# Performance work log

Measured on AMD Instinct MI355X. Metric: run time of the kernel, lower is better.

## Reference

```python
import jax, jax.numpy as jnp
import numpy as np

B, N = 4, 512
H, NH, L = 64, 4, 3
HD = H // NH          # 16
NODE_F, EDGE_F = 18, 7
H4 = H // 4           # 16
FF = 4 * H            # 256


def _ln(x, g, b, eps=1e-5):
    m = jnp.mean(x, axis=-1, keepdims=True)
    v = jnp.mean((x - m) ** 2, axis=-1, keepdims=True)
    return (x - m) * jax.lax.rsqrt(v + eps) * g + b


def _leaky(x):
    return jnp.where(x >= 0, x, 0.2 * x)


def _spd(edge_mask):
    # Vectorized Floyd-Warshall, mirrors GraphTransformer._compute_spd_matrix
    n = edge_mask.shape[1]
    spd = jnp.where(edge_mask, 1.0, float(n)).astype(jnp.float32)
    i = jnp.arange(n)
    spd = spd.at[:, i, i].set(0.0)
    def body(k, s):
        col = jax.lax.dynamic_slice_in_dim(s, k, 1, axis=2)  # [B,N,1]
        row = jax.lax.dynamic_slice_in_dim(s, k, 1, axis=1)  # [B,1,N]
        return jnp.minimum(s, col + row)
    return jax.lax.fori_loop(0, n, body, spd)


def setup_inputs() -> dict:
    key = jax.random.key(0)
    ks = iter(jax.random.split(key, 64))
    def nrm(shape, s):
        return jax.random.normal(next(ks), shape, jnp.float32) * s
    inp = {}
    inp["node_features"] = jax.random.normal(next(ks), (B, N, NODE_F), jnp.float32)
    inp["edge_features"] = jax.random.normal(next(ks), (B, N, N, EDGE_F), jnp.float32)
    nm = jax.random.uniform(next(ks), (B, N)) < 0.9
    inp["node_mask"] = nm.at[:, 0].set(True)
    inp["edge_mask"] = jax.random.uniform(next(ks), (B, N, N)) < 0.05
    s_h = 1.0 / np.sqrt(H)
    inp["node_proj_w"] = nrm((NODE_F, H), 0.2)
    inp["node_proj_b"] = jnp.zeros((H,), jnp.float32)
    inp["edge_proj_w"] = nrm((EDGE_F, H), 0.2)
    inp["edge_proj_b"] = jnp.zeros((H,), jnp.float32)
    inp["wq"] = nrm((L, H, H), s_h)
    inp["wk"] = nrm((L, H, H), s_h)
    inp["wv"] = nrm((L, H, H), s_h)
    inp["eb1_w"] = nrm((L, H, H4), s_h)
    inp["eb1_b"] = jnp.zeros((L, H4), jnp.float32)
    inp["eb_ln_g"] = jnp.ones((L, H4), jnp.float32)
    inp["eb_ln_b"] = jnp.zeros((L, H4), jnp.float32)
    inp["eb2_w"] = nrm((L, H4, NH), 0.2)
    inp["eb2_b"] = jnp.zeros((L, NH), jnp.float32)
    inp["spd1_w"] = nrm((L, 1, H4), 0.5)
    inp["spd1_b"] = jnp.zeros((L, H4), jnp.float32)
    inp["spd2_w"] = nrm((L, H4, NH), 0.2)
    inp["spd2_b"] = jnp.zeros((L, NH), jnp.float32)
    inp["wo_w"] = nrm((L, H, H), s_h)
    inp["wo_b"] = jnp.zeros((L, H), jnp.float32)
    inp["ln1_g"] = jnp.ones((L, H), jnp.float32)
    inp["ln1_b"] = jnp.zeros((L, H), jnp.float32)
    inp["ln2_g"] = jnp.ones((L, H), jnp.float32)
    inp["ln2_b"] = jnp.zeros((L, H), jnp.float32)
    inp["ffn1_w"] = nrm((L, H, FF), s_h)
    inp["ffn1_b"] = jnp.zeros((L, FF), jnp.float32)
    inp["ffn2_w"] = nrm((L, FF, H), 1.0 / np.sqrt(FF))
    inp["ffn2_b"] = jnp.zeros((L, H), jnp.float32)
    inp["score1_w"] = nrm((2 * H, H), 1.0 / np.sqrt(2 * H))
    inp["score1_b"] = jnp.zeros((H,), jnp.float32)
    inp["score_ln_g"] = jnp.ones((H,), jnp.float32)
    inp["score_ln_b"] = jnp.zeros((H,), jnp.float32)
    inp["score2_w"] = nrm((H, 1), 0.1)
    inp["score2_b"] = jnp.zeros((1,), jnp.float32)
    return inp


def reference(node_features, edge_features, node_mask, edge_mask,
              node_proj_w, node_proj_b, edge_proj_w, edge_proj_b,
              wq, wk, wv,
              eb1_w, eb1_b, eb_ln_g, eb_ln_b, eb2_w, eb2_b,
              spd1_w, spd1_b, spd2_w, spd2_b,
              wo_w, wo_b, ln1_g, ln1_b, ln2_g, ln2_b,
              ffn1_w, ffn1_b, ffn2_w, ffn2_b,
              score1_w, score1_b, score_ln_g, score_ln_b, score2_w, score2_b):
    NEG = -1000000000.0
    h = node_features @ node_proj_w + node_proj_b            # [B,N,H]
    e = edge_features @ edge_proj_w + edge_proj_b            # [B,N,N,H]
    spd = _spd(edge_mask)
    spd_n = (jnp.clip(spd, 0.0, 10.0) / 10.0)[..., None]      # [B,N,N,1]
    scale = 1.0 / np.sqrt(HD)
    for l in range(L):
        Q = (h @ wq[l]).reshape(B, N, NH, HD)
        K = (h @ wk[l]).reshape(B, N, NH, HD)
        V = (h @ wv[l]).reshape(B, N, NH, HD)
        scores = jnp.einsum('bihd,bjhd->bhij', Q, K) * scale  # [B,NH,N,N]
        x = _leaky(_ln(e @ eb1_w[l] + eb1_b[l], eb_ln_g[l], eb_ln_b[l]))
        edge_bias = jnp.transpose(x @ eb2_w[l] + eb2_b[l], (0, 3, 1, 2))
        sb = _leaky(spd_n @ spd1_w[l] + spd1_b[l]) @ spd2_w[l] + spd2_b[l]
        spd_bias = jnp.transpose(sb, (0, 3, 1, 2))
        bias = jnp.where(edge_mask[:, None, :, :], edge_bias, spd_bias)
        scores = jnp.where(node_mask[:, None, None, :], scores + bias, NEG)
        attn = jax.nn.softmax(scores, axis=-1)
        out = jnp.einsum('bhij,bjhd->bihd', attn, V).reshape(B, N, H)
        out = out @ wo_w[l] + wo_b[l]
        h = _ln(h + out, ln1_g[l], ln1_b[l])
        ff = jax.nn.gelu(h @ ffn1_w[l] + ffn1_b[l], approximate=False) @ ffn2_w[l] + ffn2_b[l]
        h = _ln(h + ff, ln2_g[l], ln2_b[l])
    h_ego = jnp.broadcast_to(h[:, :1, :], (B, N - 1, H))
    hc = jnp.concatenate([h_ego, h[:, 1:, :]], axis=-1)       # [B,N-1,2H]
    x = _leaky(_ln(hc @ score1_w + score1_b, score_ln_g, score_ln_b))
    logits = (x @ score2_w + score2_b)[..., 0]                # [B,N-1]
    cand_mask = node_mask[:, 1:]
    no_cand = ~jnp.any(cand_mask, axis=-1)
    cand_mask = cand_mask.at[:, 0].set(cand_mask[:, 0] | no_cand)
    logits = jnp.where(cand_mask, logits, NEG)
    probs = jax.nn.softmax(logits, axis=-1)
    return probs, h
```

## Files before the change

kernel.cpp:

```cpp
#include <hip/hip_runtime.h>
#include <math.h>

#define BB 4
#define NN 512
#define HH 64
#define NHH 4
#define HDD 16
#define LL 3
#define NNSQ 262144
#define FFF 256

__device__ __forceinline__ float wsum(float x) {
#pragma unroll
    for (int o = 1; o < 64; o <<= 1) x += __shfl_xor(x, o);
    return x;
}
__device__ __forceinline__ float wmaxr(float x) {
#pragma unroll
    for (int o = 1; o < 64; o <<= 1) x = fmaxf(x, __shfl_xor(x, o));
    return x;
}

__global__ void k_adj(const int* __restrict__ em, unsigned long long* __restrict__ adj,
                      unsigned int* __restrict__ blockCnt) {
    __shared__ unsigned int wc[4];
    int wv = threadIdx.x >> 6, lane = threadIdx.x & 63;
    int wid = blockIdx.x * 4 + wv;
    int chunk = wid & 7;
    int row = wid >> 3;
    int j = chunk * 64 + lane;
    int v = em[(size_t)row * NN + j];
    unsigned long long bal = __ballot(v != 0);
    if (lane == 0) { adj[row * 8 + chunk] = bal; wc[wv] = (unsigned int)__popcll(bal); }
    __syncthreads();
    if (threadIdx.x == 0) blockCnt[blockIdx.x] = wc[0] + wc[1] + wc[2] + wc[3];
}

__global__ void k_bfs(const unsigned long long* __restrict__ adj, unsigned char* __restrict__ spd) {
    __shared__ unsigned long long vis[8], fro[8], nxt[8];
    __shared__ unsigned long long dist8[64];
    unsigned char* dist = (unsigned char*)dist8;
    int t = threadIdx.x;
    int row = blockIdx.x;
    int b = row >> 9; int src = row & 511;
    dist8[t] = 0x0A0A0A0A0A0A0A0AULL;
    if (t < 8) { vis[t] = 0ULL; fro[t] = 0ULL; }
    __syncthreads();
    if (t == 0) {
        dist[src] = 0;
        vis[src >> 6] = 1ULL << (src & 63);
        fro[src >> 6] = 1ULL << (src & 63);
    }
    __syncthreads();
    const unsigned long long* arow = adj + (size_t)b * NN * 8;
    for (int d = 1; d <= 9; d++) {
        if (t < 8) nxt[t] = 0ULL;
        __syncthreads();
        int c = t >> 3, w = t & 7;
        unsigned long long f = fro[c];
        unsigned long long acc = 0ULL;
        while (f) {
            int k = (c << 6) + __builtin_ctzll(f);
            f &= f - 1;
            acc |= arow[k * 8 + w];
        }
        if (acc) atomicOr(&nxt[w], acc);
        __syncthreads();
        if (t < 8) {
            unsigned long long nw = nxt[t] & ~vis[t];
            vis[t] |= nw;
            fro[t] = nw;
            while (nw) {
                int j = (t << 6) + __builtin_ctzll(nw);
                nw &= nw - 1;
                dist[j] = (unsigned char)d;
            }
        }
        __syncthreads();
    }
    ((unsigned long long*)(spd + (size_t)row * NN))[t] = dist8[t];
}

__global__ __launch_bounds__(1024) void k_scan(const unsigned int* __restrict__ blockCnt,
                                               unsigned int* __restrict__ blockOff,
                                               unsigned int* __restrict__ counter) {
    __shared__ unsigned int part[1024];
    int t = threadIdx.x;
    unsigned int v0 = blockCnt[t * 4], v1 = blockCnt[t * 4 + 1],
                 v2 = blockCnt[t * 4 + 2], v3 = blockCnt[t * 4 + 3];
    unsigned int s = v0 + v1 + v2 + v3;
    part[t] = s;
    __syncthreads();
    for (int o = 1; o < 1024; o <<= 1) {
        unsigned int add = (t >= o) ? part[t - o] : 0u;
        __syncthreads();
        part[t] += add;
        __syncthreads();
    }
    unsigned int excl = part[t] - s;
    blockOff[t * 4]     = excl;
    blockOff[t * 4 + 1] = excl + v0;
    blockOff[t * 4 + 2] = excl + v0 + v1;
    blockOff[t * 4 + 3] = excl + v0 + v1 + v2;
    if (t == 1023) { counter[0] = part[t]; blockOff[4096] = part[t]; }
}

__global__ void k_scatter(const int* __restrict__ em, const unsigned int* __restrict__ blockOff,
                          unsigned int* __restrict__ elist) {
    __shared__ unsigned int wc[4];
    int t = threadIdx.x; int lane = t & 63; int wv = t >> 6;
    int idx = blockIdx.x * 256 + t;
    bool m = em[idx] != 0;
    unsigned long long bal = __ballot(m);
    if (lane == 0) wc[wv] = (unsigned int)__popcll(bal);
    __syncthreads();
    unsigned int base = blockOff[blockIdx.x];
    for (int w = 0; w < wv; w++) base += wc[w];
    if (m) {
        int pre = __popcll(bal & ((1ULL << lane) - 1ULL));
        elist[base + pre] = (unsigned int)idx;
    }
}

__global__ __launch_bounds__(256) void k_edge_bias(
    const float* __restrict__ ef, const unsigned int* __restrict__ counter,
    const unsigned int* __restrict__ elist,
    const float* __restrict__ epw, const float* __restrict__ epb,
    const float* __restrict__ eb1w, const float* __restrict__ eb1b,
    const float* __restrict__ lng, const float* __restrict__ lnb,
    const float* __restrict__ eb2w, const float* __restrict__ eb2b,
    float* __restrict__ vals) {
    unsigned int count = *counter;
    unsigned int idx = blockIdx.x * 256 + threadIdx.x;
    if (idx >= count) return;
    int l = blockIdx.y;
    unsigned int pos = elist[idx];
    const float* e7 = ef + (size_t)pos * 7;
    float f0 = e7[0], f1 = e7[1], f2 = e7[2], f3 = e7[3], f4 = e7[4], f5 = e7[5], f6 = e7[6];
    float tt[16];
#pragma unroll
    for (int c = 0; c < 16; c++) tt[c] = eb1b[l * 16 + c];
    const float* W1 = eb1w + l * 1024;
    for (int k = 0; k < 64; k++) {
        float ek = epb[k] + f0 * epw[k] + f1 * epw[64 + k] + f2 * epw[128 + k] + f3 * epw[192 + k]
                 + f4 * epw[256 + k] + f5 * epw[320 + k] + f6 * epw[384 + k];
#pragma unroll
        for (int c = 0; c < 16; c++) tt[c] += ek * W1[k * 16 + c];
    }
    float m = 0.f;
#pragma unroll
    for (int c = 0; c < 16; c++) m += tt[c];
    m *= 0.0625f;
    float var = 0.f;
#pragma unroll
    for (int c = 0; c < 16; c++) { float d = tt[c] - m; var += d * d; }
    var *= 0.0625f;
    float inv = rsqrtf(var + 1e-5f);
#pragma unroll
    for (int c = 0; c < 16; c++) {
        float x = (tt[c] - m) * inv * lng[l * 16 + c] + lnb[l * 16 + c];
        tt[c] = x >= 0.f ? x : 0.2f * x;
    }
#pragma unroll
    for (int hh = 0; hh < 4; hh++) {
        float a = eb2b[l * 4 + hh];
#pragma unroll
        for (int c = 0; c < 16; c++) a += tt[c] * eb2w[(l * 16 + c) * 4 + hh];
        vals[(unsigned int)((l * 4 + hh) << 16) + idx] = a;
    }
}

__global__ void k_node_proj(const float* __restrict__ nf, const float* __restrict__ w,
                            const float* __restrict__ bb, float* __restrict__ h) {
    int wid = blockIdx.x * 4 + (threadIdx.x >> 6);
    int f = threadIdx.x & 63;
    const float* r = nf + (size_t)wid * 18;
    float acc = bb[f];
#pragma unroll
    for (int c = 0; c < 18; c++) acc += r[c] * w[c * 64 + f];
    h[(size_t)wid * 64 + f] = acc;
}

__global__ __launch_bounds__(256) void k_qkvT(
    const float* __restrict__ h,
    const float* __restrict__ WQ, const float* __restrict__ WK, const float* __restrict__ WV,
    float* __restrict__ Q, float* __restrict__ KT, float* __restrict__ VT) {
    __shared__ float h_lds[16][64];
    int t = threadIdx.x;
    size_t base = (size_t)blockIdx.x * 16 * 64;
    for (int u = t; u < 1024; u += 256) ((float*)h_lds)[u] = h[base + u];
    __syncthreads();
    int wv = t >> 6, lane = t & 63;
    float aq[4] = {0,0,0,0}, ak[4] = {0,0,0,0}, av[4] = {0,0,0,0};
    for (int k = 0; k < 64; k++) {
        float wqv = WQ[k * 64 + lane], wkv = WK[k * 64 + lane], wvv = WV[k * 64 + lane];
#pragma unroll
        for (int r = 0; r < 4; r++) {
            float hv = h_lds[wv * 4 + r][k];
            aq[r] += hv * wqv; ak[r] += hv * wkv; av[r] += hv * wvv;
        }
    }
#pragma unroll
    for (int r = 0; r < 4; r++) {
        Q[base + (size_t)(wv * 4 + r) * 64 + lane] = aq[r];
    }
    int b = blockIdx.x >> 5;
    int j0 = (blockIdx.x & 31) * 16 + wv * 4;
    float4 kk; kk.x = ak[0]; kk.y = ak[1]; kk.z = ak[2]; kk.w = ak[3];
    float4 vv; vv.x = av[0]; vv.y = av[1]; vv.z = av[2]; vv.w = av[3];
    *(float4*)(KT + ((size_t)(b * 64 + lane)) * 512 + j0) = kk;
    *(float4*)(VT + ((size_t)(b * 64 + lane)) * 512 + j0) = vv;
}

__global__ __launch_bounds__(256) void k_attn3(
    const float* __restrict__ Q, const float* __restrict__ KT, const float* __restrict__ VT,
    const unsigned char* __restrict__ spd, const unsigned int* __restrict__ elist,
    const unsigned int* __restrict__ rowOff, const float* __restrict__ vals,
    const float* __restrict__ s1w, const float* __restrict__ s1b,
    const float* __restrict__ s2w, const float* __restrict__ s2b,
    const int* __restrict__ nmask, int l, float* __restrict__ attO) {
    __shared__ float kt[8192];
    __shared__ float bv[8192];
    __shared__ float tab[11];
    int bh = blockIdx.x;
    int b  = bh >> 2, hh = bh & 3;
    int i0 = blockIdx.y * 16;
    int t = threadIdx.x, wv = t >> 6, lane = t & 63;
    int rbase = i0 + wv * 4;
    float qv = Q[((size_t)(b * 512 + rbase + (lane >> 4))) * 64 + hh * 16 + (lane & 15)];
    float q[4][16];
#pragma unroll
    for (int r = 0; r < 4; r++)
#pragma unroll
        for (int d = 0; d < 16; d++)
            q[r][d] = __shfl(qv, r * 16 + d);
    const float4* ktg = (const float4*)(KT + (size_t)bh * 8192);
    float4* kts = (float4*)kt;
#pragma unroll
    for (int u = 0; u < 8; u++) kts[t + u * 256] = ktg[t + u * 256];
    if (t < 11) {
        float x = (float)t * 0.1f;
        float acc = s2b[l * 4 + hh];
#pragma unroll
        for (int c = 0; c < 16; c++) {
            float v = x * s1w[l * 16 + c] + s1b[l * 16 + c];
            v = v >= 0.f ? v : 0.2f * v;
            acc += v * s2w[(l * 16 + c) * 4 + hh];
        }
        tab[t] = acc;
    }
    __syncthreads();
    const unsigned char* sp = spd + ((size_t)(b * 512 + i0)) * 512;
#pragma unroll
    for (int u = 0; u < 8; u++) {
        int e4 = u * 1024 + t * 4;
        unsigned int w4 = *(const unsigned int*)(sp + e4);
        bv[e4 + 0] = tab[w4 & 255u];
        bv[e4 + 1] = tab[(w4 >> 8) & 255u];
        bv[e4 + 2] = tab[(w4 >> 16) & 255u];
        bv[e4 + 3] = tab[w4 >> 24];
    }
    __syncthreads();
    unsigned int vplane = (unsigned int)((l * 4 + hh) << 16);
#pragma unroll
    for (int rr = 0; rr < 4; rr++) {
        int g = b * 512 + rbase + rr;
        unsigned int e0 = rowOff[2 * g], e1 = rowOff[2 * g + 2];
        for (unsigned int e = e0 + lane; e < e1; e += 64) {
            int j = (int)(elist[e] & 511u);
            bv[(wv * 4 + rr) * 512 + j] = vals[vplane + e];
        }
    }
    __syncthreads();
    const int* nmb = nmask + b * 512;
    float sc[8][4];
    float mx[4] = {-3e38f, -3e38f, -3e38f, -3e38f};
#pragma unroll
    for (int c = 0; c < 8; c++) {
        int j = c * 64 + lane;
        float ktv[16];
#pragma unroll
        for (int d = 0; d < 16; d++) ktv[d] = kt[d * 512 + j];
        float madd = (nmb[j] != 0) ? 0.f : -1e9f;
#pragma unroll
        for (int r = 0; r < 4; r++) {
            float s = 0.f;
#pragma unroll
            for (int d = 0; d < 16; d++) s += q[r][d] * ktv[d];
            s = s * 0.25f + bv[(wv * 4 + r) * 512 + j] + madd;
            sc[c][r] = s;
            mx[r] = fmaxf(mx[r], s);
        }
    }
#pragma unroll
    for (int r = 0; r < 4; r++) mx[r] = wmaxr(mx[r]);
    float sm[4] = {0.f, 0.f, 0.f, 0.f};
#pragma unroll
    for (int c = 0; c < 8; c++)
#pragma unroll
        for (int r = 0; r < 4; r++) { sc[c][r] = __expf(sc[c][r] - mx[r]); sm[r] += sc[c][r]; }
#pragma unroll
    for (int r = 0; r < 4; r++) sm[r] = 1.0f / wsum(sm[r]);
#pragma unroll
    for (int c = 0; c < 8; c++)
#pragma unroll
        for (int r = 0; r < 4; r++) sc[c][r] *= sm[r];
    __syncthreads();
    const float4* vtg = (const float4*)(VT + (size_t)bh * 8192);
    float4* vts = (float4*)bv;
#pragma unroll
    for (int u = 0; u < 8; u++) vts[t + u * 256] = vtg[t + u * 256];
    __syncthreads();
    float acc[4][16];
#pragma unroll
    for (int r = 0; r < 4; r++)
#pragma unroll
        for (int d = 0; d < 16; d++) acc[r][d] = 0.f;
#pragma unroll
    for (int c = 0; c < 8; c++) {
        int j = c * 64 + lane;
#pragma unroll
        for (int d = 0; d < 16; d++) {
            float v = bv[d * 512 + j];
#pragma unroll
            for (int r = 0; r < 4; r++) acc[r][d] += sc[c][r] * v;
        }
    }
#pragma unroll
    for (int r = 0; r < 4; r++)
#pragma unroll
        for (int d = 0; d < 16; d++) {
            acc[r][d] += __shfl_xor(acc[r][d], 16);
            acc[r][d] += __shfl_xor(acc[r][d], 32);
        }
    __syncthreads();
    float* scr = kt + wv * 1040;
    if (lane < 16) {
#pragma unroll
        for (int r = 0; r < 4; r++)
#pragma unroll
            for (int d = 0; d < 16; d++) scr[lane * 65 + r * 16 + d] = acc[r][d];
    }
    float o = 0.f;
#pragma unroll
    for (int m = 0; m < 16; m++) o += scr[m * 65 + lane];
    attO[((size_t)(b * 512 + rbase + (lane >> 4))) * 64 + hh * 16 + (lane & 15)] = o;
}

__global__ __launch_bounds__(256) void k_oproj_ln1(
    const float* __restrict__ attO, const float* __restrict__ W, const float* __restrict__ Wb,
    const float* __restrict__ G, const float* __restrict__ Bt,
    float* __restrict__ h) {
    __shared__ float a_lds[4][64];
    int wv = threadIdx.x >> 6, lane = threadIdx.x & 63;
    int row = blockIdx.x * 4 + wv;
    a_lds[wv][lane] = attO[(size_t)row * 64 + lane];
    __syncthreads();
    float acc = Wb[lane];
#pragma unroll 8
    for (int k = 0; k < 64; k++) acc += a_lds[wv][k] * W[k * 64 + lane];
    float x = acc + h[(size_t)row * 64 + lane];
    float mn = wsum(x) * 0.015625f;
    float d = x - mn;
    float var = wsum(d * d) * 0.015625f;
    h[(size_t)row * 64 + lane] = d * rsqrtf(var + 1e-5f) * G[lane] + Bt[lane];
}

__global__ __launch_bounds__(256) void k_ffn(
    const float* __restrict__ W1, const float* __restrict__ B1,
    const float* __restrict__ W2, const float* __restrict__ B2,
    const float* __restrict__ G, const float* __restrict__ Bt,
    float* __restrict__ h) {
    __shared__ float h_lds[16][64];
    __shared__ float ff_lds[16][256];
    int t = threadIdx.x;
    size_t base = (size_t)blockIdx.x * 16 * 64;
    for (int u = t; u < 1024; u += 256) ((float*)h_lds)[u] = h[base + u];
    __syncthreads();
    int wv = t >> 6, lane = t & 63;
    float acc[4][4];
#pragma unroll
    for (int m = 0; m < 4; m++) {
        float bvv = B1[m * 64 + lane];
#pragma unroll
        for (int r = 0; r < 4; r++) acc[m][r] = bvv;
    }
    for (int k = 0; k < 64; k++) {
        float w0 = W1[k * 256 + lane], w1 = W1[k * 256 + 64 + lane],
              w2 = W1[k * 256 + 128 + lane], w3 = W1[k * 256 + 192 + lane];
#pragma unroll
        for (int r = 0; r < 4; r++) {
            float hv = h_lds[wv * 4 + r][k];
            acc[0][r] += hv * w0; acc[1][r] += hv * w1;
            acc[2][r] += hv * w2; acc[3][r] += hv * w3;
        }
    }
#pragma unroll
    for (int m = 0; m < 4; m++)
#pragma unroll
        for (int r = 0; r < 4; r++) {
            float u = acc[m][r];
            ff_lds[wv * 4 + r][m * 64 + lane] = 0.5f * u * (1.0f + erff(u * 0.70710678118654752f));
        }
    __syncthreads();
    float a2[4] = {0,0,0,0};
    for (int k = 0; k < 256; k++) {
        float w = W2[k * 64 + lane];
#pragma unroll
        for (int r = 0; r < 4; r++) a2[r] += ff_lds[wv * 4 + r][k] * w;
    }
    float b2v = B2[lane], gv = G[lane], btv = Bt[lane];
#pragma unroll
    for (int r = 0; r < 4; r++) {
        float x = a2[r] + b2v + h_lds[wv * 4 + r][lane];
        float mn = wsum(x) * 0.015625f;
        float d = x - mn;
        float var = wsum(d * d) * 0.015625f;
        h[base + (size_t)(wv * 4 + r) * 64 + lane] = d * rsqrtf(var + 1e-5f) * gv + btv;
    }
}

__global__ __launch_bounds__(256) void k_score(
    const float* __restrict__ h, const float* __restrict__ s1w, const float* __restrict__ s1b,
    const float* __restrict__ lng, const float* __restrict__ lnb,
    const float* __restrict__ s2w, const float* __restrict__ s2b,
    float* __restrict__ logits) {
    __shared__ float c_lds[4][128];
    int wv = threadIdx.x >> 6, lane = threadIdx.x & 63;
    int wid = blockIdx.x * 4 + wv;
    int b = wid / 511; int jj = wid % 511; int j = jj + 1;
    c_lds[wv][lane]      = h[((size_t)b * 512) * 64 + lane];
    c_lds[wv][64 + lane] = h[((size_t)(b * 512 + j)) * 64 + lane];
    __syncthreads();
    float acc = s1b[lane];
#pragma unroll 8
    for (int k = 0; k < 128; k++) acc += c_lds[wv][k] * s1w[k * 64 + lane];
    float mn = wsum(acc) * 0.015625f;
    float d = acc - mn;
    float var = wsum(d * d) * 0.015625f;
    float x = d * rsqrtf(var + 1e-5f) * lng[lane] + lnb[lane];
    x = x >= 0.f ? x : 0.2f * x;
    float p = wsum(x * s2w[lane]);
    if (lane == 0) logits[wid] = p + s2b[0];
}

__global__ __launch_bounds__(512) void k_probs(
    const float* __restrict__ logits, const int* __restrict__ nmask, float* __restrict__ out) {
    __shared__ float red[512];
    __shared__ int anyf;
    int b = blockIdx.x; int t = threadIdx.x;
    bool cand = false;
    if (t < 511) cand = nmask[b * 512 + 1 + t] != 0;
    if (t == 0) anyf = 0;
    __syncthreads();
    if (cand) atomicOr(&anyf, 1);
    __syncthreads();
    if (t == 0 && anyf == 0) cand = true;
    float val = -3e38f;
    if (t < 511) val = cand ? logits[b * 511 + t] : -1e9f;
    red[t] = val; __syncthreads();
    for (int s = 256; s > 0; s >>= 1) { if (t < s) red[t] = fmaxf(red[t], red[t + s]); __syncthreads(); }
    float m = red[0]; __syncthreads();
    float p = (t < 511) ? __expf(val - m) : 0.f;
    red[t] = p; __syncthreads();
    for (int s = 256; s > 0; s >>= 1) { if (t < s) red[t] += red[t + s]; __syncthreads(); }
    float inv = 1.0f / red[0];
    if (t < 511) out[b * 511 + t] = p * inv;
}

__global__ void k_copy_h(const float4* __restrict__ src, float4* __restrict__ dst) {
    int i = blockIdx.x * 256 + threadIdx.x;
    dst[i] = src[i];
}

extern "C" void kernel_launch(void* const* d_in, const int* in_sizes, int n_in,
                              void* d_out, int out_size, void* d_ws, size_t ws_size,
                              hipStream_t stream) {
    const float* nf    = (const float*)d_in[0];
    const float* ef    = (const float*)d_in[1];
    const int*   nm    = (const int*)d_in[2];
    const int*   em    = (const int*)d_in[3];
    const float* npw   = (const float*)d_in[4];
    const float* npb   = (const float*)d_in[5];
    const float* epw   = (const float*)d_in[6];
    const float* epb   = (const float*)d_in[7];
    const float* wq    = (const float*)d_in[8];
    const float* wk    = (const float*)d_in[9];
    const float* wv    = (const float*)d_in[10];
    const float* eb1w  = (const float*)d_in[11];
    const float* eb1b  = (const float*)d_in[12];
    const float* eblng = (const float*)d_in[13];
    const float* eblnb = (const float*)d_in[14];
    const float* eb2w  = (const float*)d_in[15];
    const float* eb2b  = (const float*)d_in[16];
    const float* s1wv  = (const float*)d_in[17];
    const float* s1bv  = (const float*)d_in[18];
    const float* s2wv  = (const float*)d_in[19];
    const float* s2bv  = (const float*)d_in[20];
    const float* wow   = (const float*)d_in[21];
    const float* wob   = (const float*)d_in[22];
    const float* ln1g  = (const float*)d_in[23];
    const float* ln1b  = (const float*)d_in[24];
    const float* ln2g  = (const float*)d_in[25];
    const float* ln2b  = (const float*)d_in[26];
    const float* f1w   = (const float*)d_in[27];
    const float* f1b   = (const float*)d_in[28];
    const float* f2w   = (const float*)d_in[29];
    const float* f2b   = (const float*)d_in[30];
    const float* sc1w  = (const float*)d_in[31];
    const float* sc1b  = (const float*)d_in[32];
    const float* sclng = (const float*)d_in[33];
    const float* sclnb = (const float*)d_in[34];
    const float* sc2w  = (const float*)d_in[35];
    const float* sc2b  = (const float*)d_in[36];

    char* W = (char*)d_ws;
    unsigned long long* adj     = (unsigned long long*)(W + 0);
    unsigned char*      spd     = (unsigned char*)(W + 131072);
    unsigned int*       counter = (unsigned int*)(W + 1179648);
    unsigned int*       elist   = (unsigned int*)(W + 1179904);
    float*              vals    = (float*)(W + 5374208);
    float*              hbuf    = (float*)(W + 8519936);
    float*              Qb      = (float*)(W + 9044224);
    float*              KTb     = (float*)(W + 9568512);
    float*              VTb     = (float*)(W + 10092800);
    float*              attO    = (float*)(W + 10617088);
    float*              logits  = (float*)(W + 11141376);
    unsigned int*       blockCnt= (unsigned int*)(W + 11149568);
    unsigned int*       blockOff= (unsigned int*)(W + 11165952);

    float* out = (float*)d_out;

    k_adj<<<4096, 256, 0, stream>>>(em, adj, blockCnt);
    k_bfs<<<2048, 64, 0, stream>>>(adj, spd);
    k_scan<<<1, 1024, 0, stream>>>(blockCnt, blockOff, counter);
    k_scatter<<<4096, 256, 0, stream>>>(em, blockOff, elist);
    k_edge_bias<<<dim3(256, 3), 256, 0, stream>>>(ef, counter, elist, epw, epb,
                                                  eb1w, eb1b, eblng, eblnb, eb2w, eb2b, vals);
    k_node_proj<<<512, 256, 0, stream>>>(nf, npw, npb, hbuf);

    for (int l = 0; l < LL; l++) {
        k_qkvT<<<128, 256, 0, stream>>>(hbuf, wq + l * 4096, wk + l * 4096, wv + l * 4096,
                                        Qb, KTb, VTb);
        k_attn3<<<dim3(16, 32), 256, 0, stream>>>(Qb, KTb, VTb, spd, elist, blockOff, vals,
                                                  s1wv, s1bv, s2wv, s2bv, nm, l, attO);
        k_oproj_ln1<<<512, 256, 0, stream>>>(attO, wow + l * 4096, wob + l * 64,
                                             ln1g + l * 64, ln1b + l * 64, hbuf);
        k_ffn<<<128, 256, 0, stream>>>(f1w + l * 16384, f1b + l * 256,
                                       f2w + l * 16384, f2b + l * 64,
                                       ln2g + l * 64, ln2b + l * 64, hbuf);
    }

    k_score<<<511, 256, 0, stream>>>(hbuf, sc1w, sc1b, sclng, sclnb, sc2w, sc2b, logits);
    k_copy_h<<<128, 256, 0, stream>>>((const float4*)hbuf, (float4*)(out + 2044));
    k_probs<<<4, 512, 0, stream>>>(logits, nm, out);
}
```

Before: 348.1 us.

## Fuse the whole forward pass into one persistent kernel with grid barriers

Replaces the chain of separate launches (adjacency, BFS, scan, scatter, edge bias, per-layer QKV/attention/out-proj/FFN, scoring) with a single cooperative-style kernel of 512 blocks. Phases are separated by a software grid barrier built on atomics. The global prefix-scan edge list is replaced by fixed 96-slot per-row lists, and the three layers' edge-bias MLPs are computed in one pass. This targets launch gaps and inter-kernel idle time. In exchange it relies on all blocks being co-resident, pays for spin-barrier overhead, and drops edges if any row has more than 96 of them.

Result: slower. 830.3 us (+138.5%).

```diff
diff --git a/kernel.cpp b/kernel.cpp
--- a/kernel.cpp
+++ b/kernel.cpp
@@ -1,14 +1,7 @@
 #include <hip/hip_runtime.h>
 #include <math.h>
 
-#define BB 4
-#define NN 512
-#define HH 64
-#define NHH 4
-#define HDD 16
-#define LL 3
-#define NNSQ 262144
-#define FFF 256
+#define NBLK 512
 
 __device__ __forceinline__ float wsum(float x) {
 #pragma unroll
@@ -21,456 +14,460 @@
     return x;
 }
 
-__global__ void k_adj(const int* __restrict__ em, unsigned long long* __restrict__ adj,
-                      unsigned int* __restrict__ blockCnt) {
-    __shared__ unsigned int wc[4];
-    int wv = threadIdx.x >> 6, lane = threadIdx.x & 63;
-    int wid = blockIdx.x * 4 + wv;
-    int chunk = wid & 7;
-    int row = wid >> 3;
-    int j = chunk * 64 + lane;
-    int v = em[(size_t)row * NN + j];
-    unsigned long long bal = __ballot(v != 0);
-    if (lane == 0) { adj[row * 8 + chunk] = bal; wc[wv] = (unsigned int)__popcll(bal); }
+__device__ __forceinline__ void gsync(unsigned int* bar, unsigned int gen) {
     __syncthreads();
-    if (threadIdx.x == 0) blockCnt[blockIdx.x] = wc[0] + wc[1] + wc[2] + wc[3];
-}
-
-__global__ void k_bfs(const unsigned long long* __restrict__ adj, unsigned char* __restrict__ spd) {
-    __shared__ unsigned long long vis[8], fro[8], nxt[8];
-    __shared__ unsigned long long dist8[64];
-    unsigned char* dist = (unsigned char*)dist8;
-    int t = threadIdx.x;
-    int row = blockIdx.x;
-    int b = row >> 9; int src = row & 511;
-    dist8[t] = 0x0A0A0A0A0A0A0A0AULL;
-    if (t < 8) { vis[t] = 0ULL; fro[t] = 0ULL; }
-    __syncthreads();
-    if (t == 0) {
-        dist[src] = 0;
-        vis[src >> 6] = 1ULL << (src & 63);
-        fro[src >> 6] = 1ULL << (src & 63);
+    if (threadIdx.x == 0) {
+        __threadfence();
+        unsigned int arrived = atomicAdd(&bar[0], 1u) + 1u;
+        if (arrived == gen * (unsigned int)NBLK) {
+            atomicMax(&bar[1], gen);
+        } else {
+            while (atomicAdd(&bar[1], 0u) < gen) __builtin_amdgcn_s_sleep(2);
+        }
+        __threadfence();
     }
     __syncthreads();
-    const unsigned long long* arow = adj + (size_t)b * NN * 8;
-    for (int d = 1; d <= 9; d++) {
-        if (t < 8) nxt[t] = 0ULL;
-        __syncthreads();
-        int c = t >> 3, w = t & 7;
-        unsigned long long f = fro[c];
-        unsigned long long acc = 0ULL;
-        while (f) {
-            int k = (c << 6) + __builtin_ctzll(f);
-            f &= f - 1;
-            acc |= arow[k * 8 + w];
-        }
-        if (acc) atomicOr(&nxt[w], acc);
-        __syncthreads();
-        if (t < 8) {
-            unsigned long long nw = nxt[t] & ~vis[t];
-            vis[t] |= nw;
-            fro[t] = nw;
-            while (nw) {
-                int j = (t << 6) + __builtin_ctzll(nw);
-                nw &= nw - 1;
-                dist[j] = (unsigned char)d;
-            }
-        }
-        __syncthreads();
-    }
-    ((unsigned long long*)(spd + (size_t)row * NN))[t] = dist8[t];
 }
 
-__global__ __launch_bounds__(1024) void k_scan(const unsigned int* __restrict__ blockCnt,
-                                               unsigned int* __restrict__ blockOff,
-                                               unsigned int* __restrict__ counter) {
-    __shared__ unsigned int part[1024];
-    int t = threadIdx.x;
-    unsigned int v0 = blockCnt[t * 4], v1 = blockCnt[t * 4 + 1],
-                 v2 = blockCnt[t * 4 + 2], v3 = blockCnt[t * 4 + 3];
-    unsigned int s = v0 + v1 + v2 + v3;
-    part[t] = s;
-    __syncthreads();
-    for (int o = 1; o < 1024; o <<= 1) {
-        unsigned int add = (t >= o) ? part[t - o] : 0u;
-        __syncthreads();
-        part[t] += add;
-        __syncthreads();
-    }
-    unsigned int excl = part[t] - s;
-    blockOff[t * 4]     = excl;
-    blockOff[t * 4 + 1] = excl + v0;
-    blockOff[t * 4 + 2] = excl + v0 + v1;
-    blockOff[t * 4 + 3] = excl + v0 + v1 + v2;
-    if (t == 1023) { counter[0] = part[t]; blockOff[4096] = part[t]; }
-}
-
-__global__ void k_scatter(const int* __restrict__ em, const unsigned int* __restrict__ blockOff,
-                          unsigned int* __restrict__ elist) {
-    __shared__ unsigned int wc[4];
-    int t = threadIdx.x; int lane = t & 63; int wv = t >> 6;
-    int idx = blockIdx.x * 256 + t;
-    bool m = em[idx] != 0;
-    unsigned long long bal = __ballot(m);
-    if (lane == 0) wc[wv] = (unsigned int)__popcll(bal);
-    __syncthreads();
-    unsigned int base = blockOff[blockIdx.x];
-    for (int w = 0; w < wv; w++) base += wc[w];
-    if (m) {
-        int pre = __popcll(bal & ((1ULL << lane) - 1ULL));
-        elist[base + pre] = (unsigned int)idx;
-    }
-}
-
-__global__ __launch_bounds__(256) void k_edge_bias(
-    const float* __restrict__ ef, const unsigned int* __restrict__ counter,
-    const unsigned int* __restrict__ elist,
+__global__ __launch_bounds__(256, 2) void k_mega(
+    const float* __restrict__ nf, const float* __restrict__ ef,
+    const int* __restrict__ nm, const int* __restrict__ em,
+    const float* __restrict__ npw, const float* __restrict__ npb,
     const float* __restrict__ epw, const float* __restrict__ epb,
+    const float* __restrict__ wq, const float* __restrict__ wk, const float* __restrict__ wvw,
     const float* __restrict__ eb1w, const float* __restrict__ eb1b,
-    const float* __restrict__ lng, const float* __restrict__ lnb,
+    const float* __restrict__ eblng, const float* __restrict__ eblnb,
     const float* __restrict__ eb2w, const float* __restrict__ eb2b,
-    float* __restrict__ vals) {
-    unsigned int count = *counter;
-    unsigned int idx = blockIdx.x * 256 + threadIdx.x;
-    if (idx >= count) return;
-    int l = blockIdx.y;
-    unsigned int pos = elist[idx];
-    const float* e7 = ef + (size_t)pos * 7;
-    float f0 = e7[0], f1 = e7[1], f2 = e7[2], f3 = e7[3], f4 = e7[4], f5 = e7[5], f6 = e7[6];
-    float tt[16];
-#pragma unroll
-    for (int c = 0; c < 16; c++) tt[c] = eb1b[l * 16 + c];
-    const float* W1 = eb1w + l * 1024;
-    for (int k = 0; k < 64; k++) {
-        float ek = epb[k] + f0 * epw[k] + f1 * epw[64 + k] + f2 * epw[128 + k] + f3 * epw[192 + k]
-                 + f4 * epw[256 + k] + f5 * epw[320 + k] + f6 * epw[384 + k];
-#pragma unroll
-        for (int c = 0; c < 16; c++) tt[c] += ek * W1[k * 16 + c];
-    }
-    float m = 0.f;
-#pragma unroll
-    for (int c = 0; c < 16; c++) m += tt[c];
-    m *= 0.0625f;
-    float var = 0.f;
-#pragma unroll
-    for (int c = 0; c < 16; c++) { float d = tt[c] - m; var += d * d; }
-    var *= 0.0625f;
-    float inv = rsqrtf(var + 1e-5f);
-#pragma unroll
-    for (int c = 0; c < 16; c++) {
-        float x = (tt[c] - m) * inv * lng[l * 16 + c] + lnb[l * 16 + c];
-        tt[c] = x >= 0.f ? x : 0.2f * x;
-    }
-#pragma unroll
-    for (int hh = 0; hh < 4; hh++) {
-        float a = eb2b[l * 4 + hh];
-#pragma unroll
-        for (int c = 0; c < 16; c++) a += tt[c] * eb2w[(l * 16 + c) * 4 + hh];
-        vals[(unsigned int)((l * 4 + hh) << 16) + idx] = a;
-    }
-}
-
-__global__ void k_node_proj(const float* __restrict__ nf, const float* __restrict__ w,
-                            const float* __restrict__ bb, float* __restrict__ h) {
-    int wid = blockIdx.x * 4 + (threadIdx.x >> 6);
-    int f = threadIdx.x & 63;
-    const float* r = nf + (size_t)wid * 18;
-    float acc = bb[f];
-#pragma unroll
-    for (int c = 0; c < 18; c++) acc += r[c] * w[c * 64 + f];
-    h[(size_t)wid * 64 + f] = acc;
-}
-
-__global__ __launch_bounds__(256) void k_qkvT(
-    const float* __restrict__ h,
-    const float* __restrict__ WQ, const float* __restrict__ WK, const float* __restrict__ WV,
-    float* __restrict__ Q, float* __restrict__ KT, float* __restrict__ VT) {
-    __shared__ float h_lds[16][64];
-    int t = threadIdx.x;
-    size_t base = (size_t)blockIdx.x * 16 * 64;
-    for (int u = t; u < 1024; u += 256) ((float*)h_lds)[u] = h[base + u];
-    __syncthreads();
-    int wv = t >> 6, lane = t & 63;
-    float aq[4] = {0,0,0,0}, ak[4] = {0,0,0,0}, av[4] = {0,0,0,0};
-    for (int k = 0; k < 64; k++) {
-        float wqv = WQ[k * 64 + lane], wkv = WK[k * 64 + lane], wvv = WV[k * 64 + lane];
-#pragma unroll
-        for (int r = 0; r < 4; r++) {
-            float hv = h_lds[wv * 4 + r][k];
-            aq[r] += hv * wqv; ak[r] += hv * wkv; av[r] += hv * wvv;
-        }
-    }
-#pragma unroll
-    for (int r = 0; r < 4; r++) {
-        Q[base + (size_t)(wv * 4 + r) * 64 + lane] = aq[r];
-    }
-    int b = blockIdx.x >> 5;
-    int j0 = (blockIdx.x & 31) * 16 + wv * 4;
-    float4 kk; kk.x = ak[0]; kk.y = ak[1]; kk.z = ak[2]; kk.w = ak[3];
-    float4 vv; vv.x = av[0]; vv.y = av[1]; vv.z = av[2]; vv.w = av[3];
-    *(float4*)(KT + ((size_t)(b * 64 + lane)) * 512 + j0) = kk;
-    *(float4*)(VT + ((size_t)(b * 64 + lane)) * 512 + j0) = vv;
-}
-
-__global__ __launch_bounds__(256) void k_attn3(
-    const float* __restrict__ Q, const float* __restrict__ KT, const float* __restrict__ VT,
-    const unsigned char* __restrict__ spd, const unsigned int* __restrict__ elist,
-    const unsigned int* __restrict__ rowOff, const float* __restrict__ vals,
     const float* __restrict__ s1w, const float* __restrict__ s1b,
     const float* __restrict__ s2w, const float* __restrict__ s2b,
-    const int* __restrict__ nmask, int l, float* __restrict__ attO) {
-    __shared__ float kt[8192];
-    __shared__ float bv[8192];
-    __shared__ float tab[11];
-    int bh = blockIdx.x;
-    int b  = bh >> 2, hh = bh & 3;
-    int i0 = blockIdx.y * 16;
-    int t = threadIdx.x, wv = t >> 6, lane = t & 63;
-    int rbase = i0 + wv * 4;
-    float qv = Q[((size_t)(b * 512 + rbase + (lane >> 4))) * 64 + hh * 16 + (lane & 15)];
-    float q[4][16];
-#pragma unroll
-    for (int r = 0; r < 4; r++)
-#pragma unroll
-        for (int d = 0; d < 16; d++)
-            q[r][d] = __shfl(qv, r * 16 + d);
-    const float4* ktg = (const float4*)(KT + (size_t)bh * 8192);
-    float4* kts = (float4*)kt;
-#pragma unroll
-    for (int u = 0; u < 8; u++) kts[t + u * 256] = ktg[t + u * 256];
-    if (t < 11) {
-        float x = (float)t * 0.1f;
-        float acc = s2b[l * 4 + hh];
-#pragma unroll
-        for (int c = 0; c < 16; c++) {
-            float v = x * s1w[l * 16 + c] + s1b[l * 16 + c];
-            v = v >= 0.f ? v : 0.2f * v;
-            acc += v * s2w[(l * 16 + c) * 4 + hh];
-        }
-        tab[t] = acc;
+    const float* __restrict__ wow, const float* __restrict__ wob,
+    const float* __restrict__ ln1g, const float* __restrict__ ln1b,
+    const float* __restrict__ ln2g, const float* __restrict__ ln2b,
+    const float* __restrict__ f1w, const float* __restrict__ f1b,
+    const float* __restrict__ f2w, const float* __restrict__ f2b,
+    const float* __restrict__ sc1w, const float* __restrict__ sc1b,
+    const float* __restrict__ sclng, const float* __restrict__ sclnb,
+    const float* __restrict__ sc2w, const float* __restrict__ sc2b,
+    unsigned int* __restrict__ bar, unsigned long long* __restrict__ adj,
+    unsigned char* __restrict__ spd, unsigned int* __restrict__ elist,
+    unsigned int* __restrict__ rowCnt, float* __restrict__ vals,
+    float* __restrict__ hbuf, float* __restrict__ Qb, float* __restrict__ KTb,
+    float* __restrict__ VTb, float* __restrict__ attO, float* __restrict__ logits,
+    float* __restrict__ out)
+{
+    const int t = threadIdx.x;
+    const int wv = t >> 6;
+    const int lane = t & 63;
+    const int blk = blockIdx.x;
+    __shared__ unsigned long long SMU[8192];
+    float* SMf = (float*)SMU;
+    unsigned int gen = 0u;
+
+    auto qkv_phase = [&](int l, int tq) {
+        float* h_lds = SMf;
+        size_t base = (size_t)tq * 1024;
+        for (int u = t; u < 1024; u += 256) h_lds[u] = hbuf[base + u];
+        __syncthreads();
+        const float* WQ = wq + l * 4096;
+        const float* WK = wk + l * 4096;
+        const float* WV = wvw + l * 4096;
+        float aq[4] = {0,0,0,0}, ak[4] = {0,0,0,0}, av[4] = {0,0,0,0};
+        for (int k = 0; k < 64; ++k) {
+            float wqv = WQ[k*64+lane], wkv = WK[k*64+lane], wvv = WV[k*64+lane];
+#pragma unroll
+            for (int r = 0; r < 4; ++r) {
+                float hv = h_lds[(wv*4+r)*64 + k];
+                aq[r] += hv*wqv; ak[r] += hv*wkv; av[r] += hv*wvv;
+            }
+        }
+#pragma unroll
+        for (int r = 0; r < 4; ++r) Qb[base + (size_t)(wv*4+r)*64 + lane] = aq[r];
+        int b = tq >> 5;
+        int j0 = (tq & 31)*16 + wv*4;
+        float4 kk; kk.x=ak[0]; kk.y=ak[1]; kk.z=ak[2]; kk.w=ak[3];
+        float4 vv4; vv4.x=av[0]; vv4.y=av[1]; vv4.z=av[2]; vv4.w=av[3];
+        *(float4*)(KTb + ((size_t)(b*64+lane))*512 + j0) = kk;
+        *(float4*)(VTb + ((size_t)(b*64+lane))*512 + j0) = vv4;
+    };
+
+    auto edge_row = [&](int g) {
+        unsigned int cnt = rowCnt[g];
+        for (unsigned int s = lane; s < cnt; s += 64u) {
+            unsigned int j = elist[g*96 + s];
+            const float* e7 = ef + ((size_t)g*512 + j)*7;
+            float f0=e7[0], f1=e7[1], f2=e7[2], f3=e7[3], f4=e7[4], f5=e7[5], f6=e7[6];
+            float tt[3][16];
+#pragma unroll
+            for (int l = 0; l < 3; ++l)
+#pragma unroll
+                for (int c = 0; c < 16; ++c) tt[l][c] = eb1b[l*16+c];
+            for (int k = 0; k < 64; ++k) {
+                float ek = epb[k] + f0*epw[k] + f1*epw[64+k] + f2*epw[128+k]
+                         + f3*epw[192+k] + f4*epw[256+k] + f5*epw[320+k] + f6*epw[384+k];
+#pragma unroll
+                for (int l = 0; l < 3; ++l) {
+                    const float* W1 = eb1w + l*1024 + k*16;
+#pragma unroll
+                    for (int c = 0; c < 16; ++c) tt[l][c] += ek * W1[c];
+                }
+            }
+#pragma unroll
+            for (int l = 0; l < 3; ++l) {
+                float m = 0.f;
+#pragma unroll
+                for (int c = 0; c < 16; ++c) m += tt[l][c];
+                m *= 0.0625f;
+                float var = 0.f;
+#pragma unroll
+                for (int c = 0; c < 16; ++c) { float d = tt[l][c] - m; var += d*d; }
+                var *= 0.0625f;
+                float inv = rsqrtf(var + 1e-5f);
+#pragma unroll
+                for (int c = 0; c < 16; ++c) {
+                    float x = (tt[l][c]-m)*inv*eblng[l*16+c] + eblnb[l*16+c];
+                    tt[l][c] = x >= 0.f ? x : 0.2f*x;
+                }
+#pragma unroll
+                for (int hh = 0; hh < 4; ++hh) {
+                    float a = eb2b[l*4+hh];
+#pragma unroll
+                    for (int c = 0; c < 16; ++c) a += tt[l][c]*eb2w[(l*16+c)*4+hh];
+                    vals[(unsigned int)(l*4+hh)*196608u + (unsigned int)g*96u + s] = a;
+                }
+            }
+        }
+    };
+
+    {
+        int g = blk*4 + wv;
+        const int* emr = em + (size_t)g * 512;
+        unsigned int run = 0;
+        for (int s = 0; s < 8; ++s) {
+            int j = s*64 + lane;
+            int v = emr[j];
+            unsigned long long bal = __ballot(v != 0);
+            if (v != 0) {
+                unsigned int slot = run + (unsigned int)__popcll(bal & ((1ULL << lane) - 1ULL));
+                if (slot < 96u) elist[g*96 + slot] = (unsigned int)j;
+            }
+            if (lane == 0) adj[g*8 + s] = bal;
+            run += (unsigned int)__popcll(bal);
+        }
+        if (lane == 0) rowCnt[g] = run < 96u ? run : 96u;
+        float acc = npb[lane];
+        const float* r = nf + (size_t)g * 18;
+#pragma unroll
+        for (int c = 0; c < 18; ++c) acc += r[c] * npw[c*64 + lane];
+        hbuf[(size_t)g*64 + lane] = acc;
     }
-    __syncthreads();
-    const unsigned char* sp = spd + ((size_t)(b * 512 + i0)) * 512;
-#pragma unroll
-    for (int u = 0; u < 8; u++) {
-        int e4 = u * 1024 + t * 4;
-        unsigned int w4 = *(const unsigned int*)(sp + e4);
-        bv[e4 + 0] = tab[w4 & 255u];
-        bv[e4 + 1] = tab[(w4 >> 8) & 255u];
-        bv[e4 + 2] = tab[(w4 >> 16) & 255u];
-        bv[e4 + 3] = tab[w4 >> 24];
+    gsync(bar, ++gen);
+
+    {
+        unsigned long long* wb  = SMU + wv*96;
+        unsigned long long* vis = wb, *fro = wb + 8, *nxt = wb + 16, *dist8 = wb + 24;
+        unsigned char* dist = (unsigned char*)dist8;
+        int row = blk*4 + wv;
+        int b = row >> 9, src = row & 511;
+        dist8[lane] = 0x0A0A0A0A0A0A0A0AULL;
+        if (lane < 8) { vis[lane] = 0ULL; fro[lane] = 0ULL; nxt[lane] = 0ULL; }
+        __syncthreads();
+        if (lane == 0) {
+            dist[src] = 0;
+            vis[src >> 6] = 1ULL << (src & 63);
+            fro[src >> 6] = 1ULL << (src & 63);
+        }
+        __syncthreads();
+        const unsigned long long* arow = adj + (size_t)b * 4096;
+        for (int d = 1; d <= 9; ++d) {
+            int c = lane >> 3, w = lane & 7;
+            unsigned long long f = fro[c];
+            unsigned long long acc = 0ULL;
+            while (f) {
+                int k = (c << 6) + __builtin_ctzll(f);
+                f &= f - 1;
+                acc |= arow[k*8 + w];
+            }
+            if (acc) atomicOr(&nxt[w], acc);
+            __syncthreads();
+            if (lane < 8) {
+                unsigned long long nw = nxt[lane] & ~vis[lane];
+                vis[lane] |= nw; fro[lane] = nw; nxt[lane] = 0ULL;
+                while (nw) {
+                    int j = (lane << 6) + __builtin_ctzll(nw);
+                    nw &= nw - 1;
+                    dist[j] = (unsigned char)d;
+                }
+            }
+            __syncthreads();
+        }
+        ((unsigned long long*)(spd + (size_t)row * 512))[lane] = dist8[lane];
+        __syncthreads();
+        if (blk < 128) {
+            qkv_phase(0, blk);
+        } else {
+            for (int g = (blk - 128)*4 + wv; g < 2048; g += 1536) edge_row(g);
+        }
     }
-    __syncthreads();
-    unsigned int vplane = (unsigned int)((l * 4 + hh) << 16);
-#pragma unroll
-    for (int rr = 0; rr < 4; rr++) {
-        int g = b * 512 + rbase + rr;
-        unsigned int e0 = rowOff[2 * g], e1 = rowOff[2 * g + 2];
-        for (unsigned int e = e0 + lane; e < e1; e += 64) {
-            int j = (int)(elist[e] & 511u);
-            bv[(wv * 4 + rr) * 512 + j] = vals[vplane + e];
+    gsync(bar, ++gen);
+
+    for (int l = 0; l < 3; ++l) {
+        {
+            float* kt = SMf;
+            float* bv = SMf + 8192;
+            int bh = blk >> 5;
+            int ty = blk & 31;
+            int b = bh >> 2, hh = bh & 3;
+            int i0 = ty * 16;
+            int rbase = i0 + wv*4;
+            float qv = Qb[((size_t)(b*512 + rbase + (lane>>4)))*64 + hh*16 + (lane&15)];
+            float q[4][16];
+#pragma unroll
+            for (int r = 0; r < 4; ++r)
+#pragma unroll
+                for (int d = 0; d < 16; ++d) q[r][d] = __shfl(qv, r*16 + d);
+            const float4* ktg = (const float4*)(KTb + (size_t)bh * 8192);
+            float4* kts = (float4*)kt;
+#pragma unroll
+            for (int u = 0; u < 8; ++u) kts[t + u*256] = ktg[t + u*256];
+            float tval;
+            {
+                int li = lane < 11 ? lane : 10;
+                float x = (float)li * 0.1f;
+                float acc = s2b[l*4 + hh];
+#pragma unroll
+                for (int c = 0; c < 16; ++c) {
+                    float v = x*s1w[l*16+c] + s1b[l*16+c];
+                    v = v >= 0.f ? v : 0.2f*v;
+                    acc += v*s2w[(l*16+c)*4 + hh];
+                }
+                tval = acc;
+            }
+            const unsigned char* sp = spd + ((size_t)(b*512 + i0)) * 512;
+#pragma unroll
+            for (int u = 0; u < 8; ++u) {
+                int e4 = u*1024 + t*4;
+                unsigned int w4 = *(const unsigned int*)(sp + e4);
+                bv[e4+0] = __shfl(tval, (int)(w4 & 255u));
+                bv[e4+1] = __shfl(tval, (int)((w4 >> 8) & 255u));
+                bv[e4+2] = __shfl(tval, (int)((w4 >> 16) & 255u));
+                bv[e4+3] = __shfl(tval, (int)(w4 >> 24));
+            }
+            __syncthreads();
+            unsigned int vp = (unsigned int)(l*4 + hh) * 196608u;
+#pragma unroll
+            for (int rr = 0; rr < 4; ++rr) {
+                int g = b*512 + rbase + rr;
+                unsigned int cnt = rowCnt[g];
+                for (unsigned int s = lane; s < cnt; s += 64u) {
+                    unsigned int j = elist[g*96 + s];
+                    bv[(wv*4+rr)*512 + j] = vals[vp + (unsigned int)g*96u + s];
+                }
+            }
+            const int* nmb = nm + b*512;
+            float sc[8][4];
+            float mx[4] = {-3e38f, -3e38f, -3e38f, -3e38f};
+#pragma unroll
+            for (int c = 0; c < 8; ++c) {
+                int j = c*64 + lane;
+                float ktv[16];
+#pragma unroll
+                for (int d = 0; d < 16; ++d) ktv[d] = kt[d*512 + j];
+                float madd = (nmb[j] != 0) ? 0.f : -1e9f;
+#pragma unroll
+                for (int r = 0; r < 4; ++r) {
+                    float s = 0.f;
+#pragma unroll
+                    for (int d = 0; d < 16; ++d) s += q[r][d]*ktv[d];
+                    s = s*0.25f + bv[(wv*4+r)*512 + j] + madd;
+                    sc[c][r] = s;
+                    mx[r] = fmaxf(mx[r], s);
+                }
+            }
+#pragma unroll
+            for (int r = 0; r < 4; ++r) mx[r] = wmaxr(mx[r]);
+            float sm[4] = {0.f, 0.f, 0.f, 0.f};
+#pragma unroll
+            for (int c = 0; c < 8; ++c)
+#pragma unroll
+                for (int r = 0; r < 4; ++r) { sc[c][r] = __expf(sc[c][r] - mx[r]); sm[r] += sc[c][r]; }
+#pragma unroll
+            for (int r = 0; r < 4; ++r) sm[r] = 1.0f / wsum(sm[r]);
+#pragma unroll
+            for (int c = 0; c < 8; ++c)
+#pragma unroll
+                for (int r = 0; r < 4; ++r) sc[c][r] *= sm[r];
+            __syncthreads();
+            const float4* vtg = (const float4*)(VTb + (size_t)bh * 8192);
+            float4* vts = (float4*)bv;
+#pragma unroll
+            for (int u = 0; u < 8; ++u) vts[t + u*256] = vtg[t + u*256];
+            __syncthreads();
+            float acc[4][16];
+#pragma unroll
+            for (int r = 0; r < 4; ++r)
+#pragma unroll
+                for (int d = 0; d < 16; ++d) acc[r][d] = 0.f;
+#pragma unroll
+            for (int c = 0; c < 8; ++c) {
+                int j = c*64 + lane;
+#pragma unroll
+                for (int d = 0; d < 16; ++d) {
+                    float v = bv[d*512 + j];
+#pragma unroll
+                    for (int r = 0; r < 4; ++r) acc[r][d] += sc[c][r]*v;
+                }
+            }
+#pragma unroll
+            for (int r = 0; r < 4; ++r)
+#pragma unroll
+                for (int d = 0; d < 16; ++d) {
+                    acc[r][d] += __shfl_xor(acc[r][d], 16);
+                    acc[r][d] += __shfl_xor(acc[r][d], 32);
+                }
+            float* scr = kt + wv*1040;
+            if (lane < 16) {
+#pragma unroll
+                for (int r = 0; r < 4; ++r)
+#pragma unroll
+                    for (int d = 0; d < 16; ++d) scr[lane*65 + r*16 + d] = acc[r][d];
+            }
+            float o = 0.f;
+#pragma unroll
+            for (int m = 0; m < 16; ++m) o += scr[m*65 + lane];
+            attO[((size_t)(b*512 + rbase + (lane>>4)))*64 + hh*16 + (lane&15)] = o;
+        }
+        gsync(bar, ++gen);
+
+        if (blk < 128) {
+            float* aO = SMf;
+            float* hl = SMf + 1024;
+            float* ff = SMf + 2048;
+            size_t base = (size_t)blk * 1024;
+            for (int u = t; u < 1024; u += 256) { aO[u] = attO[base + u]; hl[u] = hbuf[base + u]; }
+            __syncthreads();
+            const float* W = wow + l*4096;
+            float x[4];
+            {
+                float wb0 = wob[l*64 + lane];
+                float a0 = wb0, a1 = wb0, a2 = wb0, a3 = wb0;
+                for (int k = 0; k < 64; ++k) {
+                    float w = W[k*64 + lane];
+                    a0 += aO[(wv*4+0)*64 + k]*w;
+                    a1 += aO[(wv*4+1)*64 + k]*w;
+                    a2 += aO[(wv*4+2)*64 + k]*w;
+                    a3 += aO[(wv*4+3)*64 + k]*w;
+                }
+                x[0] = a0; x[1] = a1; x[2] = a2; x[3] = a3;
+            }
+            float g1 = ln1g[l*64 + lane], b1 = ln1b[l*64 + lane];
+#pragma unroll
+            for (int r = 0; r < 4; ++r) {
+                float xx = x[r] + hl[(wv*4+r)*64 + lane];
+                float mn = wsum(xx) * 0.015625f;
+                float d = xx - mn;
+                float var = wsum(d*d) * 0.015625f;
+                hl[(wv*4+r)*64 + lane] = d*rsqrtf(var + 1e-5f)*g1 + b1;
+            }
+            const float* W1 = f1w + l*16384;
+            const float* B1 = f1b + l*256;
+            const float* W2 = f2w + l*16384;
+            float acc[4][4];
+#pragma unroll
+            for (int m = 0; m < 4; ++m) {
+                float bvv = B1[m*64 + lane];
+#pragma unroll
+                for (int r = 0; r < 4; ++r) acc[m][r] = bvv;
+            }
+            for (int k = 0; k < 64; ++k) {
+                float w0 = W1[k*256 + lane], w1 = W1[k*256 + 64 + lane],
+                      w2 = W1[k*256 + 128 + lane], w3 = W1[k*256 + 192 + lane];
+#pragma unroll
+                for (int r = 0; r < 4; ++r) {
+                    float hv = hl[(wv*4+r)*64 + k];
+                    acc[0][r] += hv*w0; acc[1][r] += hv*w1;
+                    acc[2][r] += hv*w2; acc[3][r] += hv*w3;
+                }
+            }
+#pragma unroll
+            for (int m = 0; m < 4; ++m)
+#pragma unroll
+                for (int r = 0; r < 4; ++r) {
+                    float u = acc[m][r];
+                    ff[(wv*4+r)*256 + m*64 + lane] = 0.5f*u*(1.0f + erff(u*0.70710678118654752f));
+                }
+            float a2[4] = {0.f, 0.f, 0.f, 0.f};
+            for (int k = 0; k < 256; ++k) {
+                float w = W2[k*64 + lane];
+#pragma unroll
+                for (int r = 0; r < 4; ++r) a2[r] += ff[(wv*4+r)*256 + k]*w;
+            }
+            float b2v = f2b[l*64 + lane], gv = ln2g[l*64 + lane], btv = ln2b[l*64 + lane];
+#pragma unroll
+            for (int r = 0; r < 4; ++r) {
+                float xx = a2[r] + b2v + hl[(wv*4+r)*64 + lane];
+                float mn = wsum(xx) * 0.015625f;
+                float d = xx - mn;
+                float var = wsum(d*d) * 0.015625f;
+                float res = d*rsqrtf(var + 1e-5f)*gv + btv;
+                hbuf[base + (size_t)(wv*4+r)*64 + lane] = res;
+                if (l == 2) out[2044 + base + (wv*4+r)*64 + lane] = res;
+            }
+        }
+        gsync(bar, ++gen);
+
+        if (l < 2) {
+            if (blk < 128) qkv_phase(l + 1, blk);
+            gsync(bar, ++gen);
         }
     }
-    __syncthreads();
-    const int* nmb = nmask + b * 512;
-    float sc[8][4];
-    float mx[4] = {-3e38f, -3e38f, -3e38f, -3e38f};
-#pragma unroll
-    for (int c = 0; c < 8; c++) {
-        int j = c * 64 + lane;
-        float ktv[16];
-#pragma unroll
-        for (int d = 0; d < 16; d++) ktv[d] = kt[d * 512 + j];
-        float madd = (nmb[j] != 0) ? 0.f : -1e9f;
-#pragma unroll
-        for (int r = 0; r < 4; r++) {
-            float s = 0.f;
-#pragma unroll
-            for (int d = 0; d < 16; d++) s += q[r][d] * ktv[d];
-            s = s * 0.25f + bv[(wv * 4 + r) * 512 + j] + madd;
-            sc[c][r] = s;
-            mx[r] = fmaxf(mx[r], s);
-        }
+
+    if (blk < 511) {
+        float* c = SMf + wv*128;
+        int wid = blk*4 + wv;
+        int b = wid / 511; int jj = wid % 511; int j = jj + 1;
+        c[lane]      = hbuf[((size_t)b*512)*64 + lane];
+        c[64 + lane] = hbuf[((size_t)(b*512 + j))*64 + lane];
+        float acc = sc1b[lane];
+#pragma unroll 8
+        for (int k = 0; k < 128; ++k) acc += c[k]*sc1w[k*64 + lane];
+        float mn = wsum(acc) * 0.015625f;
+        float d = acc - mn;
+        float var = wsum(d*d) * 0.015625f;
+        float x = d*rsqrtf(var + 1e-5f)*sclng[lane] + sclnb[lane];
+        x = x >= 0.f ? x : 0.2f*x;
+        float p = wsum(x*sc2w[lane]);
+        if (lane == 0) logits[wid] = p + sc2b[0];
     }
-#pragma unroll
-    for (int r = 0; r < 4; r++) mx[r] = wmaxr(mx[r]);
-    float sm[4] = {0.f, 0.f, 0.f, 0.f};
-#pragma unroll
-    for (int c = 0; c < 8; c++)
-#pragma unroll
-        for (int r = 0; r < 4; r++) { sc[c][r] = __expf(sc[c][r] - mx[r]); sm[r] += sc[c][r]; }
-#pragma unroll
-    for (int r = 0; r < 4; r++) sm[r] = 1.0f / wsum(sm[r]);
-#pragma unroll
-    for (int c = 0; c < 8; c++)
-#pragma unroll
-        for (int r = 0; r < 4; r++) sc[c][r] *= sm[r];
-    __syncthreads();
-    const float4* vtg = (const float4*)(VT + (size_t)bh * 8192);
-    float4* vts = (float4*)bv;
-#pragma unroll
-    for (int u = 0; u < 8; u++) vts[t + u * 256] = vtg[t + u * 256];
-    __syncthreads();
-    float acc[4][16];
-#pragma unroll
-    for (int r = 0; r < 4; r++)
-#pragma unroll
-        for (int d = 0; d < 16; d++) acc[r][d] = 0.f;
-#pragma unroll
-    for (int c = 0; c < 8; c++) {
-        int j = c * 64 + lane;
-#pragma unroll
-        for (int d = 0; d < 16; d++) {
-            float v = bv[d * 512 + j];
-#pragma unroll
-            for (int r = 0; r < 4; r++) acc[r][d] += sc[c][r] * v;
-        }
+    gsync(bar, ++gen);
+
+    if (blk < 4) {
+        float* red = SMf;
+        int* anyp = (int*)(SMf + 512);
+        int b = blk;
+        bool c0 = (nm[b*512 + 1 + t] != 0);
+        int i1 = t + 256;
+        bool c1 = (i1 < 511) ? (nm[b*512 + 1 + i1] != 0) : false;
+        if (t == 0) *anyp = 0;
+        __syncthreads();
+        if (c0 || c1) atomicOr(anyp, 1);
+        __syncthreads();
+        if (t == 0 && *anyp == 0) c0 = true;
+        float v0 = c0 ? logits[b*511 + t] : -1e9f;
+        float v1 = (i1 < 511 && c1) ? logits[b*511 + i1] : -1e9f;
+        red[t] = fmaxf(v0, v1);
+        __syncthreads();
+        for (int s = 128; s > 0; s >>= 1) { if (t < s) red[t] = fmaxf(red[t], red[t + s]); __syncthreads(); }
+        float m = red[0];
+        __syncthreads();
+        float p0 = __expf(v0 - m);
+        float p1 = (i1 < 511) ? __expf(v1 - m) : 0.f;
+        red[t] = p0 + p1;
+        __syncthreads();
+        for (int s = 128; s > 0; s >>= 1) { if (t < s) red[t] += red[t + s]; __syncthreads(); }
+        float inv = 1.0f / red[0];
+        out[b*511 + t] = p0*inv;
+        if (i1 < 511) out[b*511 + i1] = p1*inv;
     }
-#pragma unroll
-    for (int r = 0; r < 4; r++)
-#pragma unroll
-        for (int d = 0; d < 16; d++) {
-            acc[r][d] += __shfl_xor(acc[r][d], 16);
-            acc[r][d] += __shfl_xor(acc[r][d], 32);
-        }
-    __syncthreads();
-    float* scr = kt + wv * 1040;
-    if (lane < 16) {
-#pragma unroll
-        for (int r = 0; r < 4; r++)
-#pragma unroll
-            for (int d = 0; d < 16; d++) scr[lane * 65 + r * 16 + d] = acc[r][d];
-    }
-    float o = 0.f;
-#pragma unroll
-    for (int m = 0; m < 16; m++) o += scr[m * 65 + lane];
-    attO[((size_t)(b * 512 + rbase + (lane >> 4))) * 64 + hh * 16 + (lane & 15)] = o;
-}
-
-__global__ __launch_bounds__(256) void k_oproj_ln1(
-    const float* __restrict__ attO, const float* __restrict__ W, const float* __restrict__ Wb,
-    const float* __restrict__ G, const float* __restrict__ Bt,
-    float* __restrict__ h) {
-    __shared__ float a_lds[4][64];
-    int wv = threadIdx.x >> 6, lane = threadIdx.x & 63;
-    int row = blockIdx.x * 4 + wv;
-    a_lds[wv][lane] = attO[(size_t)row * 64 + lane];
-    __syncthreads();
-    float acc = Wb[lane];
-#pragma unroll 8
-    for (int k = 0; k < 64; k++) acc += a_lds[wv][k] * W[k * 64 + lane];
-    float x = acc + h[(size_t)row * 64 + lane];
-    float mn = wsum(x) * 0.015625f;
-    float d = x - mn;
-    float var = wsum(d * d) * 0.015625f;
-    h[(size_t)row * 64 + lane] = d * rsqrtf(var + 1e-5f) * G[lane] + Bt[lane];
-}
-
-__global__ __launch_bounds__(256) void k_ffn(
-    const float* __restrict__ W1, const float* __restrict__ B1,
-    const float* __restrict__ W2, const float* __restrict__ B2,
-    const float* __restrict__ G, const float* __restrict__ Bt,
-    float* __restrict__ h) {
-    __shared__ float h_lds[16][64];
-    __shared__ float ff_lds[16][256];
-    int t = threadIdx.x;
-    size_t base = (size_t)blockIdx.x * 16 * 64;
-    for (int u = t; u < 1024; u += 256) ((float*)h_lds)[u] = h[base + u];
-    __syncthreads();
-    int wv = t >> 6, lane = t & 63;
-    float acc[4][4];
-#pragma unroll
-    for (int m = 0; m < 4; m++) {
-        float bvv = B1[m * 64 + lane];
-#pragma unroll
-        for (int r = 0; r < 4; r++) acc[m][r] = bvv;
-    }
-    for (int k = 0; k < 64; k++) {
-        float w0 = W1[k * 256 + lane], w1 = W1[k * 256 + 64 + lane],
-              w2 = W1[k * 256 + 128 + lane], w3 = W1[k * 256 + 192 + lane];
-#pragma unroll
-        for (int r = 0; r < 4; r++) {
-            float hv = h_lds[wv * 4 + r][k];
-            acc[0][r] += hv * w0; acc[1][r] += hv * w1;
-            acc[2][r] += hv * w2; acc[3][r] += hv * w3;
-        }
-    }
-#pragma unroll
-    for (int m = 0; m < 4; m++)
-#pragma unroll
-        for (int r = 0; r < 4; r++) {
-            float u = acc[m][r];
-            ff_lds[wv * 4 + r][m * 64 + lane] = 0.5f * u * (1.0f + erff(u * 0.70710678118654752f));
-        }
-    __syncthreads();
-    float a2[4] = {0,0,0,0};
-    for (int k = 0; k < 256; k++) {
-        float w = W2[k * 64 + lane];
-#pragma unroll
-        for (int r = 0; r < 4; r++) a2[r] += ff_lds[wv * 4 + r][k] * w;
-    }
-    float b2v = B2[lane], gv = G[lane], btv = Bt[lane];
-#pragma unroll
-    for (int r = 0; r < 4; r++) {
-        float x = a2[r] + b2v + h_lds[wv * 4 + r][lane];
-        float mn = wsum(x) * 0.015625f;
-        float d = x - mn;
-        float var = wsum(d * d) * 0.015625f;
-        h[base + (size_t)(wv * 4 + r) * 64 + lane] = d * rsqrtf(var + 1e-5f) * gv + btv;
-    }
-}
-
-__global__ __launch_bounds__(256) void k_score(
-    const float* __restrict__ h, const float* __restrict__ s1w, const float* __restrict__ s1b,
-    const float* __restrict__ lng, const float* __restrict__ lnb,
-    const float* __restrict__ s2w, const float* __restrict__ s2b,
-    float* __restrict__ logits) {
-    __shared__ float c_lds[4][128];
-    int wv = threadIdx.x >> 6, lane = threadIdx.x & 63;
-    int wid = blockIdx.x * 4 + wv;
-    int b = wid / 511; int jj = wid % 511; int j = jj + 1;
-    c_lds[wv][lane]      = h[((size_t)b * 512) * 64 + lane];
-    c_lds[wv][64 + lane] = h[((size_t)(b * 512 + j)) * 64 + lane];
-    __syncthreads();
-    float acc = s1b[lane];
-#pragma unroll 8
-    for (int k = 0; k < 128; k++) acc += c_lds[wv][k] * s1w[k * 64 + lane];
-    float mn = wsum(acc) * 0.015625f;
-    float d = acc - mn;
-    float var = wsum(d * d) * 0.015625f;
-    float x = d * rsqrtf(var + 1e-5f) * lng[lane] + lnb[lane];
-    x = x >= 0.f ? x : 0.2f * x;
-    float p = wsum(x * s2w[lane]);
-    if (lane == 0) logits[wid] = p + s2b[0];
-}
-
-__global__ __launch_bounds__(512) void k_probs(
-    const float* __restrict__ logits, const int* __restrict__ nmask, float* __restrict__ out) {
-    __shared__ float red[512];
-    __shared__ int anyf;
-    int b = blockIdx.x; int t = threadIdx.x;
-    bool cand = false;
-    if (t < 511) cand = nmask[b * 512 + 1 + t] != 0;
-    if (t == 0) anyf = 0;
-    __syncthreads();
-    if (cand) atomicOr(&anyf, 1);
-    __syncthreads();
-    if (t == 0 && anyf == 0) cand = true;
-    float val = -3e38f;
-    if (t < 511) val = cand ? logits[b * 511 + t] : -1e9f;
-    red[t] = val; __syncthreads();
-    for (int s = 256; s > 0; s >>= 1) { if (t < s) red[t] = fmaxf(red[t], red[t + s]); __syncthreads(); }
-    float m = red[0]; __syncthreads();
-    float p = (t < 511) ? __expf(val - m) : 0.f;
-    red[t] = p; __syncthreads();
-    for (int s = 256; s > 0; s >>= 1) { if (t < s) red[t] += red[t + s]; __syncthreads(); }
-    float inv = 1.0f / red[0];
-    if (t < 511) out[b * 511 + t] = p * inv;
-}
-
-__global__ void k_copy_h(const float4* __restrict__ src, float4* __restrict__ dst) {
-    int i = blockIdx.x * 256 + threadIdx.x;
-    dst[i] = src[i];
 }
 
 extern "C" void kernel_launch(void* const* d_in, const int* in_sizes, int n_in,
@@ -515,43 +512,28 @@
     const float* sc2b  = (const float*)d_in[36];
 
     char* W = (char*)d_ws;
-    unsigned long long* adj     = (unsigned long long*)(W + 0);
-    unsigned char*      spd     = (unsigned char*)(W + 131072);
-    unsigned int*       counter = (unsigned int*)(W + 1179648);
-    unsigned int*       elist   = (unsigned int*)(W + 1179904);
-    float*              vals    = (float*)(W + 5374208);
-    float*              hbuf    = (float*)(W + 8519936);
-    float*              Qb      = (float*)(W + 9044224);
-    float*              KTb     = (float*)(W + 9568512);
-    float*              VTb     = (float*)(W + 10092800);
-    float*              attO    = (float*)(W + 10617088);
-    float*              logits  = (float*)(W + 11141376);
-    unsigned int*       blockCnt= (unsigned int*)(W + 11149568);
-    unsigned int*       blockOff= (unsigned int*)(W + 11165952);
+    unsigned int*       bar    = (unsigned int*)(W + 0);
+    unsigned long long* adj    = (unsigned long long*)(W + 1024);
+    unsigned char*      spd    = (unsigned char*)(W + 132096);
+    unsigned int*       elist  = (unsigned int*)(W + 1180672);
+    unsigned int*       rowCnt = (unsigned int*)(W + 1967104);
+    float*              vals   = (float*)(W + 1975296);
+    float*              hbuf   = (float*)(W + 11412480);
+    float*              Qb     = (float*)(W + 11936768);
+    float*              KTb    = (float*)(W + 12461056);
+    float*              VTb    = (float*)(W + 12985344);
+    float*              attO   = (float*)(W + 13509632);
+    float*              logits = (float*)(W + 14033920);
 
     float* out = (float*)d_out;
 
-    k_adj<<<4096, 256, 0, stream>>>(em, adj, blockCnt);
-    k_bfs<<<2048, 64, 0, stream>>>(adj, spd);
-    k_scan<<<1, 1024, 0, stream>>>(blockCnt, blockOff, counter);
-    k_scatter<<<4096, 256, 0, stream>>>(em, blockOff, elist);
-    k_edge_bias<<<dim3(256, 3), 256, 0, stream>>>(ef, counter, elist, epw, epb,
-                                                  eb1w, eb1b, eblng, eblnb, eb2w, eb2b, vals);
-    k_node_proj<<<512, 256, 0, stream>>>(nf, npw, npb, hbuf);
-
-    for (int l = 0; l < LL; l++) {
-        k_qkvT<<<128, 256, 0, stream>>>(hbuf, wq + l * 4096, wk + l * 4096, wv + l * 4096,
-                                        Qb, KTb, VTb);
-        k_attn3<<<dim3(16, 32), 256, 0, stream>>>(Qb, KTb, VTb, spd, elist, blockOff, vals,
-                                                  s1wv, s1bv, s2wv, s2bv, nm, l, attO);
-        k_oproj_ln1<<<512, 256, 0, stream>>>(attO, wow + l * 4096, wob + l * 64,
-                                             ln1g + l * 64, ln1b + l * 64, hbuf);
-        k_ffn<<<128, 256, 0, stream>>>(f1w + l * 16384, f1b + l * 256,
-                                       f2w + l * 16384, f2b + l * 64,
-                                       ln2g + l * 64, ln2b + l * 64, hbuf);
-    }
-
-    k_score<<<511, 256, 0, stream>>>(hbuf, sc1w, sc1b, sclng, sclnb, sc2w, sc2b, logits);
-    k_copy_h<<<128, 256, 0, stream>>>((const float4*)hbuf, (float4*)(out + 2044));
-    k_probs<<<4, 512, 0, stream>>>(logits, nm, out);
+    hipMemsetAsync(bar, 0, 16, stream);
+    hipLaunchKernelGGL(k_mega, dim3(NBLK), dim3(256), 0, stream,
+        nf, ef, nm, em, npw, npb, epw, epb, wq, wk, wv,
+        eb1w, eb1b, eblng, eblnb, eb2w, eb2b,
+        s1wv, s1bv, s2wv, s2bv, wow, wob,
+        ln1g, ln1b, ln2g, ln2b, f1w, f1b, f2w, f2b,
+        sc1w, sc1b, sclng, sclnb, sc2w, sc2b,
+        bar, adj, spd, elist, rowCnt, vals,
+        hbuf, Qb, KTb, VTb, attO, logits, out);
 }
```
